# Optimization experiments

Measured on AMD Instinct MI355X. Metric: run time of the kernel, lower is better.

## Reference

```python
import jax, jax.numpy as jnp
import numpy as np

B, L1, L2, D = 16, 512, 512, 512
H, INNER = 8, 1024
HD = INNER // H  # 128

def _glorot(key, shape):
    fan_in, fan_out = shape[-2], shape[-1]
    lim = jnp.sqrt(6.0 / (fan_in + fan_out))
    return jax.random.uniform(key, shape, jnp.float32, -lim, lim)

def setup_inputs() -> dict:
    key = jax.random.key(0)
    ks = jax.random.split(key, 8)
    return {
        "primary": jax.random.normal(ks[0], (B, L1, D), jnp.float32),
        "secondary": jax.random.normal(ks[1], (B, L2, D), jnp.float32),
        "primary_mask": jnp.ones((B, L1), jnp.float32),
        "secondary_mask": jnp.ones((B, L2), jnp.float32),
        "W_aff": _glorot(ks[2], (H, D, D)),          # per-head bilinear affinity weights
        "W_p": _glorot(ks[3], (D, INNER)),            # linear_primary (no bias)
        "W_s": _glorot(ks[4], (D, INNER)),            # linear_secondary (no bias)
        "W_fp": _glorot(ks[5], (D + HD, D)),          # ffn_primary
        "b_fp": jnp.zeros((D,), jnp.float32),
        "W_fs": _glorot(ks[6], (D + HD, D)),          # ffn_secondary
        "b_fs": jnp.zeros((D,), jnp.float32),
    }

def reference(primary, secondary, primary_mask, secondary_mask,
              W_aff, W_p, W_s, W_fp, b_fp, W_fs, b_fs):
    b, l1, d = primary.shape
    l2 = secondary.shape[1]
    h = W_aff.shape[0]
    hd = W_p.shape[1] // h
    # affinity mask: (B, 1, L1, L2)
    mask = (primary_mask[:, :, None] * secondary_mask[:, None, :])[:, None, :, :]
    # multi-head bilinear affinity: tanh(P Wk S^T) -> (B, H, L1, L2)
    aff = jnp.tanh(jnp.einsum('bie,hef,bjf->bhij', primary, W_aff, secondary)) * mask
    # project + split heads -> (B, H, L, hd)
    pp = (primary @ W_p).reshape(b, l1, h, hd).transpose(0, 2, 1, 3)
    ps = (secondary @ W_s).reshape(b, l2, h, hd).transpose(0, 2, 1, 3)
    # weighted sums (ReLU activation)
    wp = jax.nn.relu(jnp.einsum('bhij,bhid->bhjd', aff, pp))  # (B, H, L2, hd)
    ws = jax.nn.relu(jnp.einsum('bhij,bhjd->bhid', aff, ps))  # (B, H, L1, hd)
    # GlobalMaxPool1D applied to (L, H, hd) per sample => max over heads
    pool_p = wp.max(axis=1)  # (B, L2, hd)
    pool_s = ws.max(axis=1)  # (B, L1, hd)
    out_p = jax.nn.relu(jnp.concatenate([primary, pool_s], -1) @ W_fp + b_fp)
    out_s = jax.nn.relu(jnp.concatenate([secondary, pool_p], -1) @ W_fs + b_fs)
    return out_p, out_s
```

## Files before the change

kernel.cpp:

```cpp
#include <hip/hip_runtime.h>
#include <hip/hip_bf16.h>

typedef short short8 __attribute__((ext_vector_type(8)));
typedef float f32x4 __attribute__((ext_vector_type(4)));

#define BM 128
#define BN 128

typedef const __attribute__((address_space(1))) void gas_t;
typedef __attribute__((address_space(3))) void las_t;

__device__ __forceinline__ unsigned short f2bf(float f) {
  unsigned int u = __float_as_uint(f);
  u += 0x7FFFu + ((u >> 16) & 1u);
  return (unsigned short)(u >> 16);
}

__device__ __forceinline__ float fast_tanh(float x) {
  x = fminf(fmaxf(x, -10.f), 10.f);
  float t = __builtin_amdgcn_exp2f(x * 2.8853900817779268f);
  return 1.f - 2.f * __builtin_amdgcn_rcpf(t + 1.f);
}

struct GemmP {
  const unsigned short* A;
  const unsigned short* A2;
  const unsigned short* Bm;
  void* C;
  const unsigned short* A_b;
  const unsigned short* A2_b;
  const unsigned short* Bm_b;
  void* C_b;
  const float* mask_p;
  const float* mask_s;
  const float* bias;
  const float* bias_b;
  long long sAb, sAh, sBb, sBh, sCb, sCh;
  int lda, lda2, ldb, ldc, M, N, K, Hh, kSplit, zSplit;
};

template <int TA, int EPI>
__global__ __launch_bounds__(256) void gemm_k(GemmP p) {
  constexpr int PA = (TA == 0) ? 32 : 40;
  constexpr int HSA = (TA == 0) ? 4096 : 5120;
  __shared__ __align__(16) unsigned short As[2 * HSA];
  __shared__ __align__(16) unsigned short Bs[8192];

  int z = blockIdx.z;
  const unsigned short* Abase = p.A;
  const unsigned short* A2 = p.A2;
  const unsigned short* Bbase = p.Bm;
  void* Cvp = p.C;
  const float* bias = p.bias;
  if (p.zSplit && z >= p.zSplit) {
    z -= p.zSplit;
    Abase = p.A_b; A2 = p.A2_b; Bbase = p.Bm_b; Cvp = p.C_b; bias = p.bias_b;
  }
  const int zb = z / p.Hh, zh = z % p.Hh;
  const unsigned short* A = Abase + (size_t)zb * p.sAb + (size_t)zh * p.sAh;
  const unsigned short* B = Bbase + (size_t)zb * p.sBb + (size_t)zh * p.sBh;
  const int m0 = blockIdx.x * BM, n0 = blockIdx.y * BN;
  const int tid = threadIdx.x;
  const int wid = tid >> 6, lane = tid & 63;
  const int wm = (wid >> 1) * 64, wn = (wid & 1) * 64;
  const int lrow = lane & 15, lkg = lane >> 4;

  f32x4 acc[4][4] = {};

  const int dm = tid >> 2, dkg = tid & 3;

  for (int k0 = 0; k0 < p.K; k0 += 64) {
    if (TA == 0) {
#pragma unroll
      for (int h = 0; h < 2; ++h) {
        const int kk = k0 + h * 32;
        const unsigned short* Ab = A;
        int al = p.lda, ko = kk;
        if (p.kSplit && kk >= p.kSplit) { Ab = A2; al = p.lda2; ko = kk - p.kSplit; }
#pragma unroll
        for (int q = 0; q < 2; ++q) {
          const unsigned short* src = Ab + (size_t)(m0 + q * 64 + dm) * al + (ko + dkg * 8);
          __builtin_amdgcn_global_load_lds((gas_t*)src,
                                           (las_t*)&As[h * HSA + q * 2048 + wid * 512],
                                           16, 0, 0);
        }
      }
    } else {
      const int kk = tid & 31, mg = (tid >> 5) << 4;
#pragma unroll
      for (int h = 0; h < 2; ++h) {
        const unsigned short* src = A + (size_t)(k0 + h * 32 + kk) * p.lda + (m0 + mg);
        uint4 v0 = *(const uint4*)src;
        uint4 v1 = *(const uint4*)(src + 8);
        unsigned short tmp[16];
        *(uint4*)&tmp[0] = v0;
        *(uint4*)&tmp[8] = v1;
#pragma unroll
        for (int j = 0; j < 16; ++j) As[h * HSA + (mg + j) * PA + kk] = tmp[j];
      }
    }
#pragma unroll
    for (int h = 0; h < 2; ++h)
#pragma unroll
      for (int q = 0; q < 2; ++q) {
        const unsigned short* src = B + (size_t)(n0 + q * 64 + dm) * p.ldb + (k0 + h * 32 + dkg * 8);
        __builtin_amdgcn_global_load_lds((gas_t*)src,
                                         (las_t*)&Bs[h * 4096 + q * 2048 + wid * 512],
                                         16, 0, 0);
      }
    __syncthreads();

#pragma unroll
    for (int h = 0; h < 2; ++h) {
      short8 af[4], bfv[4];
#pragma unroll
      for (int mt = 0; mt < 4; ++mt)
        af[mt] = *(const short8*)&As[h * HSA + (wm + mt * 16 + lrow) * PA + lkg * 8];
#pragma unroll
      for (int nt = 0; nt < 4; ++nt)
        bfv[nt] = *(const short8*)&Bs[h * 4096 + (wn + nt * 16 + lrow) * 32 + lkg * 8];
#pragma unroll
      for (int mt = 0; mt < 4; ++mt)
#pragma unroll
        for (int nt = 0; nt < 4; ++nt)
          acc[mt][nt] = __builtin_amdgcn_mfma_f32_16x16x32_bf16(af[mt], bfv[nt], acc[mt][nt], 0, 0, 0);
    }
    __syncthreads();
  }

  unsigned short* Cu = (unsigned short*)Cvp + (size_t)zb * p.sCb + (size_t)zh * p.sCh;
  float* Cf = (float*)Cvp + (size_t)zb * p.sCb + (size_t)zh * p.sCh;

  float mp[16], ms[4];
  if constexpr (EPI == 1) {
#pragma unroll
    for (int mt = 0; mt < 4; ++mt)
#pragma unroll
      for (int r = 0; r < 4; ++r)
        mp[mt * 4 + r] = p.mask_p[(size_t)zb * p.M + (m0 + wm + mt * 16 + lkg * 4 + r)];
#pragma unroll
    for (int nt = 0; nt < 4; ++nt)
      ms[nt] = p.mask_s[(size_t)zb * p.N + (n0 + wn + nt * 16 + lrow)];
  }
  if constexpr (EPI == 3) {
#pragma unroll
    for (int nt = 0; nt < 4; ++nt)
      ms[nt] = bias[n0 + wn + nt * 16 + lrow];
  }

#pragma unroll
  for (int mt = 0; mt < 4; ++mt) {
#pragma unroll
    for (int nt = 0; nt < 4; ++nt) {
      f32x4 a = acc[mt][nt];
#pragma unroll
      for (int r = 0; r < 4; ++r) {
        const int grow = m0 + wm + mt * 16 + lkg * 4 + r;
        const int gcol = n0 + wn + nt * 16 + lrow;
        const float v = a[r];
        if constexpr (EPI == 0) {
          Cu[(size_t)grow * p.ldc + gcol] = f2bf(v);
        } else if constexpr (EPI == 1) {
          Cu[(size_t)grow * p.ldc + gcol] = f2bf(fast_tanh(v) * (mp[mt * 4 + r] * ms[nt]));
        } else if constexpr (EPI == 2) {
          atomicMax((int*)Cf + (size_t)grow * p.ldc + gcol, __float_as_int(fmaxf(v, 0.f)));
        } else {
          Cf[(size_t)grow * p.ldc + gcol] = fmaxf(v + ms[nt], 0.f);
        }
      }
    }
  }
}

__global__ void cvt2_bf16_v4(const float4* a, const float4* b, ushort4* oa, ushort4* ob, int n4) {
  int i = blockIdx.x * 256 + threadIdx.x;
  const float4* s;
  ushort4* d;
  int j;
  if (i < n4) { s = a; d = oa; j = i; }
  else { j = i - n4; if (j >= n4) return; s = b; d = ob; }
  float4 v = s[j];
  ushort4 o;
  o.x = f2bf(v.x); o.y = f2bf(v.y); o.z = f2bf(v.z); o.w = f2bf(v.w);
  d[j] = o;
}

__global__ void cvt_bf16_v4(const float4* in, ushort4* out, int n4) {
  int i = blockIdx.x * 256 + threadIdx.x;
  if (i >= n4) return;
  float4 v = in[i];
  ushort4 o;
  o.x = f2bf(v.x); o.y = f2bf(v.y); o.z = f2bf(v.z); o.w = f2bf(v.w);
  out[i] = o;
}

__global__ __launch_bounds__(256) void trans_bf16(const float* in, unsigned short* out,
                                                  const float* in2, unsigned short* out2,
                                                  int R, int C, int zSplit) {
  __shared__ float tile[32][33];
  int z = blockIdx.z;
  const float* ib = in;
  unsigned short* ob = out;
  if (zSplit && z >= zSplit) { z -= zSplit; ib = in2; ob = out2; }
  const int r0 = blockIdx.y * 32, c0 = blockIdx.x * 32;
  const int tx = threadIdx.x & 31, ty = threadIdx.x >> 5;
  const float* src = ib + (size_t)z * R * C;
  unsigned short* dst = ob + (size_t)z * R * C;
#pragma unroll
  for (int j = 0; j < 4; ++j)
    tile[ty + j * 8][tx] = src[(size_t)(r0 + ty + j * 8) * C + (c0 + tx)];
  __syncthreads();
#pragma unroll
  for (int j = 0; j < 4; ++j)
    dst[(size_t)(c0 + ty + j * 8) * R + (r0 + tx)] = f2bf(tile[tx][ty + j * 8]);
}

template <int TA, int EPI>
static inline void run_gemm(const GemmP& q, int Z, hipStream_t stream) {
  dim3 grid(q.M / BM, q.N / BN, Z);
  gemm_k<TA, EPI><<<grid, dim3(256), 0, stream>>>(q);
}

extern "C" void kernel_launch(void* const* d_in, const int* in_sizes, int n_in,
                              void* d_out, int out_size, void* d_ws, size_t ws_size,
                              hipStream_t stream) {
  (void)in_sizes; (void)n_in; (void)out_size; (void)ws_size;
  const float* primary   = (const float*)d_in[0];
  const float* secondary = (const float*)d_in[1];
  const float* pmask     = (const float*)d_in[2];
  const float* smask     = (const float*)d_in[3];
  const float* W_aff     = (const float*)d_in[4];
  const float* W_p       = (const float*)d_in[5];
  const float* W_s       = (const float*)d_in[6];
  const float* W_fp      = (const float*)d_in[7];
  const float* b_fp      = (const float*)d_in[8];
  const float* W_fs      = (const float*)d_in[9];
  const float* b_fs      = (const float*)d_in[10];

  constexpr int Bb = 16, L = 512, Dd = 512, Hh = 8, HDd = 128, INNER = 1024, CAT = 640;
  constexpr int NT = Hh * Dd;
  constexpr long long LD = (long long)L * Dd;
  constexpr long long LL = (long long)L * L;

  char* base = (char*)d_ws;
  size_t off = 0;
  auto alloc = [&](size_t bytes) -> void* {
    void* r = base + off;
    off += (bytes + 255) & ~(size_t)255;
    return r;
  };

  unsigned short* Pbf   = (unsigned short*)alloc((size_t)Bb * L * Dd * 2);
  unsigned short* Sbf   = (unsigned short*)alloc((size_t)Bb * L * Dd * 2);
  unsigned short* WaT   = (unsigned short*)alloc((size_t)NT * Dd * 2);
  unsigned short* WpT   = (unsigned short*)alloc((size_t)INNER * Dd * 2);
  unsigned short* WsT   = (unsigned short*)alloc((size_t)INNER * Dd * 2);
  unsigned short* WfpT  = (unsigned short*)alloc((size_t)Dd * CAT * 2);
  unsigned short* WfsT  = (unsigned short*)alloc((size_t)Dd * CAT * 2);
  unsigned short* psT   = (unsigned short*)alloc((size_t)Bb * INNER * L * 2);
  unsigned short* ppT   = (unsigned short*)alloc((size_t)Bb * INNER * L * 2);
  unsigned short* Tbuf  = (unsigned short*)alloc((size_t)Bb * L * NT * 2);
  unsigned short* affb  = (unsigned short*)alloc((size_t)Bb * Hh * L * L * 2);
  float* pool_p = (float*)alloc((size_t)Bb * L * HDd * 4);
  float* pool_s = (float*)alloc((size_t)Bb * L * HDd * 4);
  unsigned short* poolPbf = (unsigned short*)alloc((size_t)Bb * L * HDd * 2);
  unsigned short* poolSbf = (unsigned short*)alloc((size_t)Bb * L * HDd * 2);

  {
    const int n4 = (Bb * L * Dd) / 4;
    cvt2_bf16_v4<<<dim3((2 * n4) / 256), dim3(256), 0, stream>>>(
        (const float4*)primary, (const float4*)secondary, (ushort4*)Pbf, (ushort4*)Sbf, n4);
  }
  trans_bf16<<<dim3(Dd / 32, Dd / 32, Hh), dim3(256), 0, stream>>>(
      W_aff, WaT, nullptr, nullptr, Dd, Dd, 0);
  trans_bf16<<<dim3(INNER / 32, Dd / 32, 2), dim3(256), 0, stream>>>(
      W_p, WpT, W_s, WsT, Dd, INNER, 1);
  trans_bf16<<<dim3(Dd / 32, CAT / 32, 2), dim3(256), 0, stream>>>(
      W_fp, WfpT, W_fs, WfsT, CAT, Dd, 1);

  hipMemsetAsync(pool_p, 0, (size_t)2 * Bb * L * HDd * 4, stream);

  {
    GemmP g{};
    g.A = Pbf; g.lda = Dd;
    g.Bm = WaT; g.ldb = Dd;
    g.C = Tbuf; g.ldc = NT;
    g.M = Bb * L; g.N = NT; g.K = Dd; g.Hh = 1;
    run_gemm<0, 0>(g, 1, stream);
  }

  {
    GemmP g{};
    g.A = WsT; g.lda = Dd; g.sAb = 0;
    g.Bm = Sbf; g.ldb = Dd; g.sBb = LD;
    g.C = psT; g.ldc = L; g.sCb = (long long)INNER * L;
    g.A_b = WpT; g.Bm_b = Pbf; g.C_b = ppT;
    g.M = INNER; g.N = L; g.K = Dd; g.Hh = 1; g.zSplit = Bb;
    run_gemm<0, 0>(g, 2 * Bb, stream);
  }

  {
    GemmP g{};
    g.A = Tbuf; g.lda = NT; g.sAb = (long long)L * NT; g.sAh = Dd;
    g.Bm = Sbf; g.ldb = Dd; g.sBb = LD; g.sBh = 0;
    g.C = affb; g.ldc = L; g.sCb = (long long)Hh * LL; g.sCh = LL;
    g.mask_p = pmask; g.mask_s = smask;
    g.M = L; g.N = L; g.K = Dd; g.Hh = Hh;
    run_gemm<0, 1>(g, Bb * Hh, stream);
  }

  {
    GemmP g{};
    g.A = affb; g.lda = L; g.sAb = (long long)Hh * LL; g.sAh = LL;
    g.Bm = psT; g.ldb = L; g.sBb = (long long)INNER * L; g.sBh = (long long)HDd * L;
    g.C = pool_s; g.ldc = HDd; g.sCb = (long long)L * HDd; g.sCh = 0;
    g.M = L; g.N = HDd; g.K = L; g.Hh = Hh;
    run_gemm<0, 2>(g, Bb * Hh, stream);
  }

  {
    GemmP g{};
    g.A = affb; g.lda = L; g.sAb = (long long)Hh * LL; g.sAh = LL;
    g.Bm = ppT; g.ldb = L; g.sBb = (long long)INNER * L; g.sBh = (long long)HDd * L;
    g.C = pool_p; g.ldc = HDd; g.sCb = (long long)L * HDd; g.sCh = 0;
    g.M = L; g.N = HDd; g.K = L; g.Hh = Hh;
    run_gemm<1, 2>(g, Bb * Hh, stream);
  }

  {
    const int n4 = (2 * Bb * L * HDd) / 4;
    cvt_bf16_v4<<<dim3((n4 + 255) / 256), dim3(256), 0, stream>>>((const float4*)pool_p, (ushort4*)poolPbf, n4);
  }

  {
    GemmP g{};
    g.A = Pbf; g.lda = Dd;
    g.A2 = poolSbf; g.lda2 = HDd; g.kSplit = Dd;
    g.Bm = WfpT; g.ldb = CAT;
    g.C = d_out; g.ldc = Dd;
    g.bias = b_fp;
    g.A_b = Sbf; g.A2_b = poolPbf; g.Bm_b = WfsT;
    g.C_b = (float*)d_out + (size_t)Bb * L * Dd;
    g.bias_b = b_fs;
    g.M = Bb * L; g.N = Dd; g.K = CAT; g.Hh = 1; g.zSplit = 1;
    run_gemm<0, 3>(g, 2, stream);
  }
}
```

Baseline: 356.7 us.

## Merge prep kernels, pair independent GEMMs, fuse pool bf16 conversion into FFN

Replaces the separate cast, transpose and memset launches with a single prep kernel that dispatches on block index. The two independent projection GEMMs and the two pooling GEMMs are each packed into one launch via a paired kernel. The final FFN GEMM now reads the fp32 pooled tensors directly and converts them to bf16 while staging into LDS, which removes the separate conversion kernel. Fewer launches and less idle tail time are traded for dynamic shared memory, a non-async load path for the second K segment, and hardcoded block counts tied to the problem shape.

```diff
diff --git a/kernel.cpp b/kernel.cpp
--- a/kernel.cpp
+++ b/kernel.cpp
@@ -24,42 +24,42 @@
 
 struct GemmP {
   const unsigned short* A;
-  const unsigned short* A2;
   const unsigned short* Bm;
   void* C;
+  const float* A2f;
   const unsigned short* A_b;
-  const unsigned short* A2_b;
   const unsigned short* Bm_b;
   void* C_b;
+  const float* A2f_b;
   const float* mask_p;
   const float* mask_s;
   const float* bias;
   const float* bias_b;
   long long sAb, sAh, sBb, sBh, sCb, sCh;
-  int lda, lda2, ldb, ldc, M, N, K, Hh, kSplit, zSplit;
+  int lda, lda2, ldb, ldc, M, N, K, Hh, kSplit, zSplit, nbx, nby;
 };
 
 template <int TA, int EPI>
-__global__ __launch_bounds__(256) void gemm_k(GemmP p) {
+__device__ __forceinline__ void gemm_body(const GemmP& p, int bx, int by, int bz, char* smem_) {
   constexpr int PA = (TA == 0) ? 32 : 40;
   constexpr int HSA = (TA == 0) ? 4096 : 5120;
-  __shared__ __align__(16) unsigned short As[2 * HSA];
-  __shared__ __align__(16) unsigned short Bs[8192];
-
-  int z = blockIdx.z;
+  unsigned short* As = (unsigned short*)smem_;
+  unsigned short* Bs = (unsigned short*)(smem_ + 2 * HSA * 2);
+
+  int z = bz;
   const unsigned short* Abase = p.A;
-  const unsigned short* A2 = p.A2;
   const unsigned short* Bbase = p.Bm;
   void* Cvp = p.C;
+  const float* A2f = p.A2f;
   const float* bias = p.bias;
   if (p.zSplit && z >= p.zSplit) {
     z -= p.zSplit;
-    Abase = p.A_b; A2 = p.A2_b; Bbase = p.Bm_b; Cvp = p.C_b; bias = p.bias_b;
+    Abase = p.A_b; Bbase = p.Bm_b; Cvp = p.C_b; A2f = p.A2f_b; bias = p.bias_b;
   }
   const int zb = z / p.Hh, zh = z % p.Hh;
   const unsigned short* A = Abase + (size_t)zb * p.sAb + (size_t)zh * p.sAh;
   const unsigned short* B = Bbase + (size_t)zb * p.sBb + (size_t)zh * p.sBh;
-  const int m0 = blockIdx.x * BM, n0 = blockIdx.y * BN;
+  const int m0 = bx * BM, n0 = by * BN;
   const int tid = threadIdx.x;
   const int wid = tid >> 6, lane = tid & 63;
   const int wm = (wid >> 1) * 64, wn = (wid & 1) * 64;
@@ -69,22 +69,50 @@
 
   const int dm = tid >> 2, dkg = tid & 3;
 
-  for (int k0 = 0; k0 < p.K; k0 += 64) {
+  auto mfma_block = [&]() {
+#pragma unroll
+    for (int h = 0; h < 2; ++h) {
+      short8 af[4], bfv[4];
+#pragma unroll
+      for (int mt = 0; mt < 4; ++mt)
+        af[mt] = *(const short8*)&As[h * HSA + (wm + mt * 16 + lrow) * PA + lkg * 8];
+#pragma unroll
+      for (int nt = 0; nt < 4; ++nt)
+        bfv[nt] = *(const short8*)&Bs[h * 4096 + (wn + nt * 16 + lrow) * 32 + lkg * 8];
+#pragma unroll
+      for (int mt = 0; mt < 4; ++mt)
+#pragma unroll
+        for (int nt = 0; nt < 4; ++nt)
+          acc[mt][nt] = __builtin_amdgcn_mfma_f32_16x16x32_bf16(af[mt], bfv[nt], acc[mt][nt], 0, 0, 0);
+    }
+  };
+  auto stage_b = [&](int k0) {
+#pragma unroll
+    for (int h = 0; h < 2; ++h)
+#pragma unroll
+      for (int q = 0; q < 2; ++q) {
+        const unsigned short* src = B + (size_t)(n0 + q * 64 + dm) * p.ldb + (k0 + h * 32 + dkg * 8);
+        __builtin_amdgcn_global_load_lds((gas_t*)src,
+                                         (las_t*)&Bs[h * 4096 + q * 2048 + wid * 512],
+                                         16, 0, 0);
+      }
+  };
+
+  const int nIter = p.K >> 6;
+  const int nIter1 = p.kSplit ? (p.kSplit >> 6) : nIter;
+
+  for (int it = 0; it < nIter1; ++it) {
+    const int k0 = it << 6;
     if (TA == 0) {
 #pragma unroll
-      for (int h = 0; h < 2; ++h) {
-        const int kk = k0 + h * 32;
-        const unsigned short* Ab = A;
-        int al = p.lda, ko = kk;
-        if (p.kSplit && kk >= p.kSplit) { Ab = A2; al = p.lda2; ko = kk - p.kSplit; }
+      for (int h = 0; h < 2; ++h)
 #pragma unroll
         for (int q = 0; q < 2; ++q) {
-          const unsigned short* src = Ab + (size_t)(m0 + q * 64 + dm) * al + (ko + dkg * 8);
+          const unsigned short* src = A + (size_t)(m0 + q * 64 + dm) * p.lda + (k0 + h * 32 + dkg * 8);
           __builtin_amdgcn_global_load_lds((gas_t*)src,
                                            (las_t*)&As[h * HSA + q * 2048 + wid * 512],
                                            16, 0, 0);
         }
-      }
     } else {
       const int kk = tid & 31, mg = (tid >> 5) << 4;
 #pragma unroll
@@ -99,33 +127,34 @@
         for (int j = 0; j < 16; ++j) As[h * HSA + (mg + j) * PA + kk] = tmp[j];
       }
     }
-#pragma unroll
-    for (int h = 0; h < 2; ++h)
-#pragma unroll
-      for (int q = 0; q < 2; ++q) {
-        const unsigned short* src = B + (size_t)(n0 + q * 64 + dm) * p.ldb + (k0 + h * 32 + dkg * 8);
-        __builtin_amdgcn_global_load_lds((gas_t*)src,
-                                         (las_t*)&Bs[h * 4096 + q * 2048 + wid * 512],
-                                         16, 0, 0);
+    stage_b(k0);
+    __syncthreads();
+    mfma_block();
+    __syncthreads();
+  }
+
+  if (TA == 0 && p.kSplit) {
+    for (int it = nIter1; it < nIter; ++it) {
+      const int k0 = it << 6;
+#pragma unroll
+      for (int h = 0; h < 2; ++h) {
+        const int ko = k0 + h * 32 - p.kSplit;
+#pragma unroll
+        for (int q = 0; q < 2; ++q) {
+          const float* src = A2f + (size_t)(m0 + q * 64 + dm) * p.lda2 + (ko + dkg * 8);
+          float4 v0 = *(const float4*)src;
+          float4 v1 = *(const float4*)(src + 4);
+          __attribute__((aligned(16))) unsigned short t[8];
+          t[0] = f2bf(v0.x); t[1] = f2bf(v0.y); t[2] = f2bf(v0.z); t[3] = f2bf(v0.w);
+          t[4] = f2bf(v1.x); t[5] = f2bf(v1.y); t[6] = f2bf(v1.z); t[7] = f2bf(v1.w);
+          *(uint4*)&As[h * HSA + (q * 64 + dm) * 32 + dkg * 8] = *(const uint4*)t;
+        }
       }
-    __syncthreads();
-
-#pragma unroll
-    for (int h = 0; h < 2; ++h) {
-      short8 af[4], bfv[4];
-#pragma unroll
-      for (int mt = 0; mt < 4; ++mt)
-        af[mt] = *(const short8*)&As[h * HSA + (wm + mt * 16 + lrow) * PA + lkg * 8];
-#pragma unroll
-      for (int nt = 0; nt < 4; ++nt)
-        bfv[nt] = *(const short8*)&Bs[h * 4096 + (wn + nt * 16 + lrow) * 32 + lkg * 8];
-#pragma unroll
-      for (int mt = 0; mt < 4; ++mt)
-#pragma unroll
-        for (int nt = 0; nt < 4; ++nt)
-          acc[mt][nt] = __builtin_amdgcn_mfma_f32_16x16x32_bf16(af[mt], bfv[nt], acc[mt][nt], 0, 0, 0);
+      stage_b(k0);
+      __syncthreads();
+      mfma_block();
+      __syncthreads();
     }
-    __syncthreads();
   }
 
   unsigned short* Cu = (unsigned short*)Cvp + (size_t)zb * p.sCb + (size_t)zh * p.sCh;
@@ -157,55 +186,48 @@
       for (int r = 0; r < 4; ++r) {
         const int grow = m0 + wm + mt * 16 + lkg * 4 + r;
         const int gcol = n0 + wn + nt * 16 + lrow;
+        const size_t idx = (size_t)grow * p.ldc + gcol;
         const float v = a[r];
         if constexpr (EPI == 0) {
-          Cu[(size_t)grow * p.ldc + gcol] = f2bf(v);
+          Cu[idx] = f2bf(v);
         } else if constexpr (EPI == 1) {
-          Cu[(size_t)grow * p.ldc + gcol] = f2bf(fast_tanh(v) * (mp[mt * 4 + r] * ms[nt]));
+          Cu[idx] = f2bf(fast_tanh(v) * (mp[mt * 4 + r] * ms[nt]));
         } else if constexpr (EPI == 2) {
-          atomicMax((int*)Cf + (size_t)grow * p.ldc + gcol, __float_as_int(fmaxf(v, 0.f)));
+          atomicMax((int*)Cf + idx, __float_as_int(fmaxf(v, 0.f)));
         } else {
-          Cf[(size_t)grow * p.ldc + gcol] = fmaxf(v + ms[nt], 0.f);
+          Cf[idx] = fmaxf(v + ms[nt], 0.f);
         }
       }
     }
   }
 }
 
-__global__ void cvt2_bf16_v4(const float4* a, const float4* b, ushort4* oa, ushort4* ob, int n4) {
-  int i = blockIdx.x * 256 + threadIdx.x;
-  const float4* s;
-  ushort4* d;
-  int j;
-  if (i < n4) { s = a; d = oa; j = i; }
-  else { j = i - n4; if (j >= n4) return; s = b; d = ob; }
-  float4 v = s[j];
-  ushort4 o;
-  o.x = f2bf(v.x); o.y = f2bf(v.y); o.z = f2bf(v.z); o.w = f2bf(v.w);
-  d[j] = o;
-}
-
-__global__ void cvt_bf16_v4(const float4* in, ushort4* out, int n4) {
-  int i = blockIdx.x * 256 + threadIdx.x;
-  if (i >= n4) return;
-  float4 v = in[i];
-  ushort4 o;
-  o.x = f2bf(v.x); o.y = f2bf(v.y); o.z = f2bf(v.z); o.w = f2bf(v.w);
-  out[i] = o;
-}
-
-__global__ __launch_bounds__(256) void trans_bf16(const float* in, unsigned short* out,
-                                                  const float* in2, unsigned short* out2,
-                                                  int R, int C, int zSplit) {
-  __shared__ float tile[32][33];
-  int z = blockIdx.z;
-  const float* ib = in;
-  unsigned short* ob = out;
-  if (zSplit && z >= zSplit) { z -= zSplit; ib = in2; ob = out2; }
-  const int r0 = blockIdx.y * 32, c0 = blockIdx.x * 32;
+template <int TA, int EPI>
+__global__ __launch_bounds__(256) void gemm_k(GemmP p) {
+  extern __shared__ char smem[];
+  gemm_body<TA, EPI>(p, blockIdx.x, blockIdx.y, blockIdx.z, smem);
+}
+
+template <int TA1, int EPI1, int TA2, int EPI2>
+__global__ __launch_bounds__(256) void gemm_pair_k(GemmP a, GemmP b, int nA) {
+  extern __shared__ char smem[];
+  int bid = blockIdx.x;
+  if (bid < nA) {
+    const int per = a.nbx * a.nby;
+    const int z = bid / per, r = bid % per;
+    gemm_body<TA1, EPI1>(a, r % a.nbx, r / a.nbx, z, smem);
+  } else {
+    bid -= nA;
+    const int per = b.nbx * b.nby;
+    const int z = bid / per, r = bid % per;
+    gemm_body<TA2, EPI2>(b, r % b.nbx, r / b.nbx, z, smem);
+  }
+}
+
+__device__ __forceinline__ void trans_body(const float* src, unsigned short* dst,
+                                           int R, int C, int bx, int by, float (*tile)[33]) {
+  const int r0 = by * 32, c0 = bx * 32;
   const int tx = threadIdx.x & 31, ty = threadIdx.x >> 5;
-  const float* src = ib + (size_t)z * R * C;
-  unsigned short* dst = ob + (size_t)z * R * C;
 #pragma unroll
   for (int j = 0; j < 4; ++j)
     tile[ty + j * 8][tx] = src[(size_t)(r0 + ty + j * 8) * C + (c0 + tx)];
@@ -215,10 +237,43 @@
     dst[(size_t)(c0 + ty + j * 8) * R + (r0 + tx)] = f2bf(tile[tx][ty + j * 8]);
 }
 
-template <int TA, int EPI>
-static inline void run_gemm(const GemmP& q, int Z, hipStream_t stream) {
-  dim3 grid(q.M / BM, q.N / BN, Z);
-  gemm_k<TA, EPI><<<grid, dim3(256), 0, stream>>>(q);
+__global__ __launch_bounds__(256) void prep_k(const float* P, const float* S,
+                                              unsigned short* Pbf, unsigned short* Sbf,
+                                              const float* W_aff, unsigned short* WaT,
+                                              const float* W_p, unsigned short* WpT,
+                                              const float* W_s, unsigned short* WsT,
+                                              const float* W_fp, unsigned short* WfpT,
+                                              const float* W_fs, unsigned short* WfsT,
+                                              float* poolz) {
+  __shared__ float tile[32][33];
+  const int bid = blockIdx.x;
+  if (bid < 8192) {
+    const int n4 = 1048576;
+    int i = bid * 256 + threadIdx.x;
+    const float4* s = (const float4*)P;
+    ushort4* d = (ushort4*)Pbf;
+    if (i >= n4) { i -= n4; s = (const float4*)S; d = (ushort4*)Sbf; }
+    float4 v = s[i];
+    ushort4 o;
+    o.x = f2bf(v.x); o.y = f2bf(v.y); o.z = f2bf(v.z); o.w = f2bf(v.w);
+    d[i] = o;
+  } else if (bid < 10240) {
+    const int l = bid - 8192;
+    const int z = l >> 8, r = l & 255;
+    trans_body(W_aff + (size_t)z * 262144, WaT + (size_t)z * 262144, 512, 512,
+               r & 15, r >> 4, tile);
+  } else if (bid < 11264) {
+    const int l = bid - 10240;
+    const int z = l >> 9, r = l & 511;
+    trans_body(z ? W_s : W_p, z ? WsT : WpT, 512, 1024, r & 31, r >> 5, tile);
+  } else if (bid < 11904) {
+    const int l = bid - 11264;
+    const int z = l / 320, r = l % 320;
+    trans_body(z ? W_fs : W_fp, z ? WfsT : WfpT, 640, 512, r & 15, r >> 4, tile);
+  } else {
+    const int i = (bid - 11904) * 256 + threadIdx.x;
+    ((float4*)poolz)[i] = float4{0.f, 0.f, 0.f, 0.f};
+  }
 }
 
 extern "C" void kernel_launch(void* const* d_in, const int* in_sizes, int n_in,
@@ -263,40 +318,26 @@
   unsigned short* affb  = (unsigned short*)alloc((size_t)Bb * Hh * L * L * 2);
   float* pool_p = (float*)alloc((size_t)Bb * L * HDd * 4);
   float* pool_s = (float*)alloc((size_t)Bb * L * HDd * 4);
-  unsigned short* poolPbf = (unsigned short*)alloc((size_t)Bb * L * HDd * 2);
-  unsigned short* poolSbf = (unsigned short*)alloc((size_t)Bb * L * HDd * 2);
+
+  prep_k<<<dim3(13952), dim3(256), 0, stream>>>(primary, secondary, Pbf, Sbf,
+                                                W_aff, WaT, W_p, WpT, W_s, WsT,
+                                                W_fp, WfpT, W_fs, WfsT, pool_p);
 
   {
-    const int n4 = (Bb * L * Dd) / 4;
-    cvt2_bf16_v4<<<dim3((2 * n4) / 256), dim3(256), 0, stream>>>(
-        (const float4*)primary, (const float4*)secondary, (ushort4*)Pbf, (ushort4*)Sbf, n4);
-  }
-  trans_bf16<<<dim3(Dd / 32, Dd / 32, Hh), dim3(256), 0, stream>>>(
-      W_aff, WaT, nullptr, nullptr, Dd, Dd, 0);
-  trans_bf16<<<dim3(INNER / 32, Dd / 32, 2), dim3(256), 0, stream>>>(
-      W_p, WpT, W_s, WsT, Dd, INNER, 1);
-  trans_bf16<<<dim3(Dd / 32, CAT / 32, 2), dim3(256), 0, stream>>>(
-      W_fp, WfpT, W_fs, WfsT, CAT, Dd, 1);
-
-  hipMemsetAsync(pool_p, 0, (size_t)2 * Bb * L * HDd * 4, stream);
-
-  {
-    GemmP g{};
-    g.A = Pbf; g.lda = Dd;
-    g.Bm = WaT; g.ldb = Dd;
-    g.C = Tbuf; g.ldc = NT;
-    g.M = Bb * L; g.N = NT; g.K = Dd; g.Hh = 1;
-    run_gemm<0, 0>(g, 1, stream);
-  }
-
-  {
-    GemmP g{};
-    g.A = WsT; g.lda = Dd; g.sAb = 0;
-    g.Bm = Sbf; g.ldb = Dd; g.sBb = LD;
-    g.C = psT; g.ldc = L; g.sCb = (long long)INNER * L;
-    g.A_b = WpT; g.Bm_b = Pbf; g.C_b = ppT;
-    g.M = INNER; g.N = L; g.K = Dd; g.Hh = 1; g.zSplit = Bb;
-    run_gemm<0, 0>(g, 2 * Bb, stream);
+    GemmP a{};
+    a.A = Pbf; a.lda = Dd;
+    a.Bm = WaT; a.ldb = Dd;
+    a.C = Tbuf; a.ldc = NT;
+    a.M = Bb * L; a.N = NT; a.K = Dd; a.Hh = 1; a.nbx = 64; a.nby = 32;
+
+    GemmP b{};
+    b.A = WsT; b.lda = Dd; b.sAb = 0;
+    b.Bm = Sbf; b.ldb = Dd; b.sBb = LD;
+    b.C = psT; b.ldc = L; b.sCb = (long long)INNER * L;
+    b.A_b = WpT; b.Bm_b = Pbf; b.C_b = ppT;
+    b.M = INNER; b.N = L; b.K = Dd; b.Hh = 1; b.zSplit = Bb; b.nbx = 8; b.nby = 4;
+
+    gemm_pair_k<0, 0, 0, 0><<<dim3(2048 + 1024), dim3(256), 32768, stream>>>(a, b, 2048);
   }
 
   {
@@ -306,43 +347,34 @@
     g.C = affb; g.ldc = L; g.sCb = (long long)Hh * LL; g.sCh = LL;
     g.mask_p = pmask; g.mask_s = smask;
     g.M = L; g.N = L; g.K = Dd; g.Hh = Hh;
-    run_gemm<0, 1>(g, Bb * Hh, stream);
+    gemm_k<0, 1><<<dim3(4, 4, Bb * Hh), dim3(256), 32768, stream>>>(g);
   }
 
   {
-    GemmP g{};
-    g.A = affb; g.lda = L; g.sAb = (long long)Hh * LL; g.sAh = LL;
-    g.Bm = psT; g.ldb = L; g.sBb = (long long)INNER * L; g.sBh = (long long)HDd * L;
-    g.C = pool_s; g.ldc = HDd; g.sCb = (long long)L * HDd; g.sCh = 0;
-    g.M = L; g.N = HDd; g.K = L; g.Hh = Hh;
-    run_gemm<0, 2>(g, Bb * Hh, stream);
-  }
-
-  {
-    GemmP g{};
-    g.A = affb; g.lda = L; g.sAb = (long long)Hh * LL; g.sAh = LL;
-    g.Bm = ppT; g.ldb = L; g.sBb = (long long)INNER * L; g.sBh = (long long)HDd * L;
-    g.C = pool_p; g.ldc = HDd; g.sCb = (long long)L * HDd; g.sCh = 0;
-    g.M = L; g.N = HDd; g.K = L; g.Hh = Hh;
-    run_gemm<1, 2>(g, Bb * Hh, stream);
-  }
-
-  {
-    const int n4 = (2 * Bb * L * HDd) / 4;
-    cvt_bf16_v4<<<dim3((n4 + 255) / 256), dim3(256), 0, stream>>>((const float4*)pool_p, (ushort4*)poolPbf, n4);
+    GemmP g4{};
+    g4.A = affb; g4.lda = L; g4.sAb = (long long)Hh * LL; g4.sAh = LL;
+    g4.Bm = psT; g4.ldb = L; g4.sBb = (long long)INNER * L; g4.sBh = (long long)HDd * L;
+    g4.C = pool_s; g4.ldc = HDd; g4.sCb = (long long)L * HDd; g4.sCh = 0;
+    g4.M = L; g4.N = HDd; g4.K = L; g4.Hh = Hh; g4.nbx = 4; g4.nby = 1;
+
+    GemmP g5 = g4;
+    g5.Bm = ppT;
+    g5.C = pool_p;
+
+    gemm_pair_k<0, 2, 1, 2><<<dim3(512 + 512), dim3(256), 36864, stream>>>(g4, g5, 512);
   }
 
   {
     GemmP g{};
     g.A = Pbf; g.lda = Dd;
-    g.A2 = poolSbf; g.lda2 = HDd; g.kSplit = Dd;
+    g.A2f = pool_s; g.lda2 = HDd; g.kSplit = Dd;
     g.Bm = WfpT; g.ldb = CAT;
     g.C = d_out; g.ldc = Dd;
     g.bias = b_fp;
-    g.A_b = Sbf; g.A2_b = poolPbf; g.Bm_b = WfsT;
+    g.A_b = Sbf; g.A2f_b = pool_p; g.Bm_b = WfsT;
     g.C_b = (float*)d_out + (size_t)Bb * L * Dd;
     g.bias_b = b_fs;
     g.M = Bb * L; g.N = Dd; g.K = CAT; g.Hh = 1; g.zSplit = 1;
-    run_gemm<0, 3>(g, 2, stream);
-  }
-}
+    gemm_k<0, 3><<<dim3(64, 4, 2), dim3(256), 32768, stream>>>(g);
+  }
+}
```

New measurement: 344.8 us. -3.3%, faster.
